# Kernel tuning notes

Hardware: AMD Instinct MI355X
Metric: run time of the kernel (lower is better)

## Reference

```python
import jax, jax.numpy as jnp
import numpy as np

N = 131072       # nodes
E = 2097152      # edges
B = 4096         # target user/item pairs (= batched subgraphs)
F_IN = 32        # dataset.num_features
H = 32           # latent dim per conv layer
L = 4            # num conv layers
R = 5            # num relations
NB = 4           # num bases
D = 256          # 2*sum(latent_dim), LSTM input/hidden size


def setup_inputs() -> dict:
    key = jax.random.key(0)
    ks = jax.random.split(key, 16)
    x = jax.random.normal(ks[0], (N, F_IN), dtype=jnp.float32)
    edge_index = jax.random.randint(ks[1], (2, E), 0, N, dtype=jnp.int32)
    edge_type = jax.random.randint(ks[2], (E,), 0, R, dtype=jnp.int32)
    user_idx = jnp.arange(B, dtype=jnp.int32)
    item_idx = jnp.arange(B, dtype=jnp.int32) + B
    s = 0.1
    basis = jax.random.normal(ks[3], (L, NB, H, H), dtype=jnp.float32) * s
    comp = jax.random.normal(ks[4], (L, R, NB), dtype=jnp.float32) * s
    root = jax.random.normal(ks[5], (L, H, H), dtype=jnp.float32) * s
    conv_bias = jnp.zeros((L, H), dtype=jnp.float32)
    w_ih = jax.random.normal(ks[6], (2, 4 * D, D), dtype=jnp.float32) * (1.0 / np.sqrt(D))
    w_hh = jax.random.normal(ks[7], (2, 4 * D, D), dtype=jnp.float32) * (1.0 / np.sqrt(D))
    b_ih = jnp.zeros((2, 4 * D), dtype=jnp.float32)
    b_hh = jnp.zeros((2, 4 * D), dtype=jnp.float32)
    lin1_w = jax.random.normal(ks[8], (128, D), dtype=jnp.float32) * (1.0 / np.sqrt(D))
    lin1_b = jnp.zeros((128,), dtype=jnp.float32)
    lin2_w = jax.random.normal(ks[9], (1, 128), dtype=jnp.float32) * (1.0 / np.sqrt(128))
    lin2_b = jnp.zeros((1,), dtype=jnp.float32)
    return dict(x=x, edge_index=edge_index, edge_type=edge_type,
                user_idx=user_idx, item_idx=item_idx,
                basis=basis, comp=comp, root=root, conv_bias=conv_bias,
                w_ih=w_ih, w_hh=w_hh, b_ih=b_ih, b_hh=b_hh,
                lin1_w=lin1_w, lin1_b=lin1_b, lin2_w=lin2_w, lin2_b=lin2_b)


def _lstm_layer(inp, w_ih_l, w_hh_l, b_ih_l, b_hh_l):
    # inp: [T, D] unbatched sequence (torch LSTM with 2D input)
    T = inp.shape[0]
    # precompute input contribution for all timesteps: [T, 4D]
    x_gates = inp @ w_ih_l.T + b_ih_l + b_hh_l

    def step(carry, xg):
        h, c = carry
        gates = xg + h @ w_hh_l.T            # [4D]
        i, f, g, o = jnp.split(gates, 4)
        i = jax.nn.sigmoid(i)
        f = jax.nn.sigmoid(f)
        g = jnp.tanh(g)
        o = jax.nn.sigmoid(o)
        c = f * c + i * g
        h = o * jnp.tanh(c)
        return (h, c), h

    h0 = jnp.zeros((D,), dtype=inp.dtype)
    (_, _), out = jax.lax.scan(step, (h0, h0), x_gates)
    return out  # [T, D]


def _forward(x, edge_index, edge_type, user_idx, item_idx,
             basis, comp, root, conv_bias,
             w_ih, w_hh, b_ih, b_hh, lin1_w, lin1_b, lin2_w, lin2_b):
    src, dst = edge_index[0], edge_index[1]
    # per-(dst, relation) mean normalization (RGCNConv aggr='mean'); same every layer
    seg = dst.astype(jnp.int32) * R + edge_type.astype(jnp.int32)  # [E]
    counts = jax.ops.segment_sum(jnp.ones((E,), jnp.float32), seg, num_segments=N * R)
    edge_norm = (1.0 / jnp.maximum(counts, 1.0))[seg]              # [E]

    h = x
    concat_states = []
    for l in range(L):
        # basis-decomposed relation weights: W_r = sum_b comp[r,b] * basis[b]
        basis_out = jnp.einsum('nd,bde->nbe', h, basis[l])         # [N, NB, H]
        comp_e = comp[l][edge_type]                                 # [E, NB]
        msg = jnp.einsum('eb,ebo->eo', comp_e, basis_out[src])      # [E, H]
        msg = msg * edge_norm[:, None]
        agg = jax.ops.segment_sum(msg, dst, num_segments=N)         # [N, H]
        h = jnp.tanh(agg + h @ root[l] + conv_bias[l])
        concat_states.append(h)
    states = jnp.concatenate(concat_states, axis=1)                 # [N, 4H] = [N,128]

    u = states[user_idx]                                            # [B, 128]
    v = states[item_idx]                                            # [B, 128]
    z = jnp.concatenate([u, v], axis=1)                             # [B, 256]

    # 2-layer LSTM over the B dimension (torch treats [B,256] as seq_len=B, unbatched)
    z = _lstm_layer(z, w_ih[0], w_hh[0], b_ih[0], b_hh[0])
    z = _lstm_layer(z, w_ih[1], w_hh[1], b_ih[1], b_hh[1])

    z = jax.nn.relu(z @ lin1_w.T + lin1_b)                          # [B, 128]
    z = z @ lin2_w.T + lin2_b                                       # [B, 1]
    return z[:, 0]


def reference(x, edge_index, edge_type, user_idx, item_idx,
              basis, comp, root, conv_bias,
              w_ih, w_hh, b_ih, b_hh, lin1_w, lin1_b, lin2_w, lin2_b):
    return _forward(x, edge_index, edge_type, user_idx, item_idx,
                    basis, comp, root, conv_bias,
                    w_ih, w_hh, b_ih, b_hh, lin1_w, lin1_b, lin2_w, lin2_b)
```

## Files before the change

kernel.cpp:

```cpp
#include <hip/hip_runtime.h>
#include <hip/hip_bf16.h>
#include <hip/hip_fp16.h>

#define N_NODES 131072
#define N_EDGES 2097152
#define BSZ     4096
#define NREL    5
#define NBASIS  4

typedef unsigned int uint;
typedef unsigned short ushort;
typedef _Float16 v2h __attribute__((ext_vector_type(2)));
typedef __attribute__((ext_vector_type(8))) short bf16x8;
typedef __attribute__((ext_vector_type(4))) float f32x4;
typedef uint u32x4v __attribute__((ext_vector_type(4)));

__device__ __forceinline__ float bflo(uint u){ union{uint i;float f;}x; x.i = u<<16; return x.f; }
__device__ __forceinline__ float bf2f(ushort u){ return bflo((uint)u); }
__device__ __forceinline__ ushort f2bf(float f){
  union{float f;uint i;}x; x.f=f;
  uint r = (x.i + 0x7fffu + ((x.i>>16)&1u)) >> 16;
  return (ushort)r;
}
__device__ __forceinline__ float sigm(float x){ return 1.0f/(1.0f+__expf(-x)); }
__device__ __forceinline__ float tanh_fast(float x){
  x = fminf(fmaxf(x,-15.f),15.f);
  float e = __expf(2.0f*x);
  return (e-1.0f)/(e+1.0f);
}
__device__ __forceinline__ float dot2h(uint a, uint b, float c){
#if __has_builtin(__builtin_amdgcn_fdot2)
  return __builtin_amdgcn_fdot2(__builtin_bit_cast(v2h,a), __builtin_bit_cast(v2h,b), c, false);
#else
  v2h ah = __builtin_bit_cast(v2h,a), bh = __builtin_bit_cast(v2h,b);
  return c + (float)ah.x*(float)bh.x + (float)ah.y*(float)bh.y;
#endif
}

__device__ __forceinline__ void store16(uint* p, u32x4v v){
  asm volatile("global_store_dwordx4 %0, %1, off sc0 sc1" :: "v"(p), "v"(v) : "memory");
}
__device__ __forceinline__ u32x4v poll16(const uint* p, uint want){
  u32x4v v;
  do {
    asm volatile("global_load_dwordx4 %0, %1, off sc0 sc1\n\ts_waitcnt vmcnt(0)"
      : "=v"(v) : "v"(p) : "memory");
  } while (v.x != want);
  return v;
}

__global__ void k_cvt_half(const float* __restrict__ in, __half* __restrict__ out, int n){
  int i = blockIdx.x*256 + threadIdx.x;
  if (i < n) out[i] = __float2half(in[i]);
}
__global__ void k_cvt_bf(const float* __restrict__ in, ushort* __restrict__ out, int n){
  int i = blockIdx.x*256 + threadIdx.x;
  if (i < n) out[i] = f2bf(in[i]);
}

__global__ void k_count(const int* __restrict__ ei, const int* __restrict__ et, int* __restrict__ cnt){
  int e = blockIdx.x*256 + threadIdx.x;
  if (e < N_EDGES){
    int d = ei[N_EDGES + e];
    int r = et[e];
    atomicAdd(&cnt[d*NREL + r], 1);
  }
}
__global__ void k_inv(float* __restrict__ buf){
  int i = blockIdx.x*256 + threadIdx.x;
  if (i < N_NODES*NREL){
    int c = ((int*)buf)[i];
    buf[i] = (c > 0) ? (1.0f/(float)c) : 1.0f;
  }
}

__global__ void k_hb(const float* __restrict__ x, const ushort* __restrict__ states, int l,
                     const float* __restrict__ basis_l, uint2* __restrict__ hb){
  __shared__ float bs[NBASIS*32*32];
  __shared__ float hs[256];
  int tid = threadIdx.x;
  #pragma unroll
  for (int r = 0; r < 16; r++){ int idx = r*256 + tid; bs[idx] = basis_l[idx]; }
  int nbase = blockIdx.x*8;
  if (l == 0){
    hs[tid] = x[nbase*32 + tid];
  } else {
    int n = nbase + (tid >> 5), i = tid & 31;
    hs[tid] = bf2f(states[n*128 + (l-1)*32 + i]);
  }
  __syncthreads();
  int nl = tid >> 5, j = tid & 31;
  float a0=0.f,a1=0.f,a2=0.f,a3=0.f;
  #pragma unroll
  for (int i = 0; i < 32; i++){
    float hv = hs[nl*32 + i];
    a0 += hv*bs[0*1024 + i*32 + j];
    a1 += hv*bs[1*1024 + i*32 + j];
    a2 += hv*bs[2*1024 + i*32 + j];
    a3 += hv*bs[3*1024 + i*32 + j];
  }
  uint2 o;
  o.x = (uint)f2bf(a0) | ((uint)f2bf(a1) << 16);
  o.y = (uint)f2bf(a2) | ((uint)f2bf(a3) << 16);
  hb[(nbase + nl)*32 + j] = o;
}

__global__ void k_edge(const int* __restrict__ ei, const int* __restrict__ et,
                       const float* __restrict__ comp_l, const float* __restrict__ inv,
                       const uint2* __restrict__ hb, float* __restrict__ agg){
  __shared__ float cl[NREL*NBASIS];
  int tid = threadIdx.x;
  if (tid < NREL*NBASIS) cl[tid] = comp_l[tid];
  __syncthreads();
  int e = blockIdx.x*8 + (tid >> 5);
  int j = tid & 31;
  int src = ei[e];
  int dst = ei[N_EDGES + e];
  int r = et[e];
  float nrm = inv[dst*NREL + r];
  uint2 v = hb[src*32 + j];
  float m = nrm*(cl[r*4+0]*bflo(v.x)       + cl[r*4+1]*bflo(v.x >> 16)
               + cl[r*4+2]*bflo(v.y)       + cl[r*4+3]*bflo(v.y >> 16));
  atomicAdd(&agg[dst*32 + j], m);
}

__global__ void k_combine(const float* __restrict__ agg, const float* __restrict__ x,
                          ushort* __restrict__ states, int l,
                          const float* __restrict__ root_l, const float* __restrict__ bias_l){
  __shared__ float rt[1024];
  __shared__ float hs[256];
  int tid = threadIdx.x;
  #pragma unroll
  for (int r = 0; r < 4; r++) rt[r*256 + tid] = root_l[r*256 + tid];
  int nbase = blockIdx.x*8;
  if (l == 0){
    hs[tid] = x[nbase*32 + tid];
  } else {
    int n = nbase + (tid >> 5), i = tid & 31;
    hs[tid] = bf2f(states[n*128 + (l-1)*32 + i]);
  }
  __syncthreads();
  int nl = tid >> 5, j = tid & 31;
  int n = nbase + nl;
  float acc = agg[n*32 + j] + bias_l[j];
  #pragma unroll
  for (int i = 0; i < 32; i++) acc += hs[nl*32 + i] * rt[i*32 + j];
  states[n*128 + l*32 + j] = f2bf(tanh_fast(acc));
}

__global__ void k_gather(const ushort* __restrict__ states, const int* __restrict__ uidx,
                         const int* __restrict__ vidx, ushort* __restrict__ z){
  int b = blockIdx.x;
  int k = threadIdx.x;
  int node = (k < 128) ? uidx[b] : vidx[b];
  z[b*256 + k] = states[node*128 + (k & 127)];
}

__global__ void k_xgemm(const ushort* __restrict__ A, const ushort* __restrict__ W,
                        const float* __restrict__ bih, const float* __restrict__ bhh,
                        float* __restrict__ xg){
  int gw = blockIdx.x*4 + (threadIdx.x >> 6);
  int lane = threadIdx.x & 63;
  int t0 = (gw >> 6)*16;
  int j0 = (gw & 63)*16;
  int m = lane & 15, q = lane >> 4;
  const ushort* ap = A + (t0 + m)*256 + q*8;
  const ushort* bp = W + (j0 + m)*256 + q*8;
  f32x4 acc = {0.f,0.f,0.f,0.f};
  #pragma unroll
  for (int kk = 0; kk < 8; kk++){
    bf16x8 a = *(const bf16x8*)(ap + kk*32);
    bf16x8 b = *(const bf16x8*)(bp + kk*32);
    acc = __builtin_amdgcn_mfma_f32_16x16x32_bf16(a, b, acc, 0, 0, 0);
  }
  int j = j0 + m;
  float bias = bih[j] + bhh[j];
  #pragma unroll
  for (int r = 0; r < 4; r++){
    int t = t0 + q*4 + r;
    xg[t*1024 + j] = acc[r] + bias;
  }
}

#define REP8J(M,q) M(q,0) M(q,1) M(q,2) M(q,3) M(q,4) M(q,5) M(q,6) M(q,7)
#define REPQ(M) REP8J(M,0) REP8J(M,1) REP8J(M,2) REP8J(M,3)
#define WDECL(q,j) uint4 W##q##_##j = wp##q[j];
#define WPIN(q,j)  asm volatile("" : "+v"(W##q##_##j.x), "+v"(W##q##_##j.y), \
                                     "+v"(W##q##_##j.z), "+v"(W##q##_##j.w));
#define DOTJ(j) { uint4 H = hp[j]; \
  a0 = dot2h(W0_##j.x, H.x, a0); b0 = dot2h(W0_##j.y, H.y, b0); \
  a0 = dot2h(W0_##j.z, H.z, a0); b0 = dot2h(W0_##j.w, H.w, b0); \
  a1 = dot2h(W1_##j.x, H.x, a1); b1 = dot2h(W1_##j.y, H.y, b1); \
  a1 = dot2h(W1_##j.z, H.z, a1); b1 = dot2h(W1_##j.w, H.w, b1); \
  a2 = dot2h(W2_##j.x, H.x, a2); b2 = dot2h(W2_##j.y, H.y, b2); \
  a2 = dot2h(W2_##j.z, H.z, a2); b2 = dot2h(W2_##j.w, H.w, b2); \
  a3 = dot2h(W3_##j.x, H.x, a3); b3 = dot2h(W3_##j.y, H.y, b3); \
  a3 = dot2h(W3_##j.z, H.z, a3); b3 = dot2h(W3_##j.w, H.w, b3); }
#define BFLY(r) { \
  float _t = __int_as_float(__builtin_amdgcn_update_dpp(0, __float_as_int(r), 0xB1, 0xF, 0xF, true)); \
  r += _t; \
  _t = __int_as_float(__builtin_amdgcn_update_dpp(0, __float_as_int(r), 0x4E, 0xF, 0xF, true)); \
  r += _t; }

__launch_bounds__(256, 1)
__global__ void k_scan4(const float* __restrict__ xg, const __half* __restrict__ whh,
                        ushort* __restrict__ outh, uint* hx){
  int b = blockIdx.x;
  if (b & 7) return;
  int g = b >> 3;
  if (g >= 4) return;
  __shared__ uint hq[2][144];
  int t = threadIdx.x;
  int w = t >> 6, lane = t & 63, qd = lane >> 2, s = lane & 3;
  int u = g*64 + w*16 + qd;
  const uint4* wp0 = (const uint4*)(whh + ((size_t)(u      ))*256 + s*64);
  const uint4* wp1 = (const uint4*)(whh + ((size_t)(u + 256))*256 + s*64);
  const uint4* wp2 = (const uint4*)(whh + ((size_t)(u + 512))*256 + s*64);
  const uint4* wp3 = (const uint4*)(whh + ((size_t)(u + 768))*256 + s*64);
  REPQ(WDECL)
  REPQ(WPIN)
  if (t < 144) hq[0][t] = 0u;
  float c = 0.f;
  float px = xg[s*256 + u];
  int pollidx = t - 64;
  int bb = (lane & 48) * 4;
  __syncthreads();
  for (int step = 0; step < 4096; step++){
    int rb = step & 1, wb = rb ^ 1;
    const uint4* hp = (const uint4*)&hq[rb][s*36];
    float a0=0.f,a1=0.f,a2=0.f,a3=0.f,b0=0.f,b1=0.f,b2=0.f,b3=0.f;
    int nstep = (step < 4095) ? step + 1 : step;
    float npx = xg[(size_t)nstep*1024 + s*256 + u];
    DOTJ(0) DOTJ(1) DOTJ(2) DOTJ(3) DOTJ(4) DOTJ(5) DOTJ(6) DOTJ(7)
    float r0 = a0 + b0, r1 = a1 + b1, r2 = a2 + b2, r3 = a3 + b3;
    r0 += (s == 0) ? px : 0.f;
    r1 += (s == 1) ? px : 0.f;
    r2 += (s == 2) ? px : 0.f;
    r3 += (s == 3) ? px : 0.f;
    BFLY(r0) BFLY(r1) BFLY(r2) BFLY(r3)
    float iv = sigm(r0), fv = sigm(r1), gv = tanh_fast(r2), ov = sigm(r3);
    c = fv*c + iv*gv;
    float hv = ov*tanh_fast(c);
    px = npx;
    uint hvh = (uint)__half_as_ushort(__float2half(hv));
    uint g0 = (uint)__builtin_amdgcn_ds_bpermute(bb +  0, (int)hvh);
    uint g1 = (uint)__builtin_amdgcn_ds_bpermute(bb + 16, (int)hvh);
    uint g2 = (uint)__builtin_amdgcn_ds_bpermute(bb + 32, (int)hvh);
    uint g3 = (uint)__builtin_amdgcn_ds_bpermute(bb + 48, (int)hvh);
    if ((lane & 15) == 0){
      int cc = w*4 + (lane >> 4);
      u32x4v ch;
      ch.x = (uint)(step + 1);
      ch.y = (g0 & 0xffffu) | (g1 << 16);
      ch.z = (g2 & 0xffffu) | (g3 << 16);
      ch.w = 0u;
      store16(hx + (((size_t)rb*4 + g)*16 + cc)*4, ch);
    }
    if (s == 0){
      ((__half*)&hq[wb][g*36])[w*16 + qd] = __ushort_as_half((ushort)hvh);
      outh[(size_t)step*256 + u] = f2bf(hv);
    }
    if ((uint)pollidx < 48u){
      int o = pollidx >> 4, cc = pollidx & 15;
      int gg = o + (o >= g);
      u32x4v v = poll16(hx + (((size_t)rb*4 + gg)*16 + cc)*4, (uint)(step + 1));
      hq[wb][gg*36 + 2*cc]     = v.y;
      hq[wb][gg*36 + 2*cc + 1] = v.z;
    }
    __syncthreads();
  }
}

__global__ void k_head1(const ushort* __restrict__ h, const float* __restrict__ w,
                        const float* __restrict__ b, float* __restrict__ out){
  __shared__ float s[256];
  int t = blockIdx.x, j = threadIdx.x;
  s[j]       = bf2f(h[t*256 + j]);
  s[j + 128] = bf2f(h[t*256 + 128 + j]);
  __syncthreads();
  float acc = b[j];
  const float4* wr4 = (const float4*)(w + j*256);
  #pragma unroll
  for (int k4 = 0; k4 < 64; k4++){
    float4 v = wr4[k4];
    int k = k4*4;
    acc += s[k+0]*v.x + s[k+1]*v.y + s[k+2]*v.z + s[k+3]*v.w;
  }
  out[t*128 + j] = fmaxf(acc, 0.f);
}
__global__ void k_head2(const float* __restrict__ hm, const float* __restrict__ w,
                        const float* __restrict__ b, float* __restrict__ out){
  int t = blockIdx.x*256 + threadIdx.x;
  if (t < BSZ){
    float acc = b[0];
    #pragma unroll
    for (int k = 0; k < 128; k++) acc += hm[t*128 + k]*w[k];
    out[t] = acc;
  }
}

extern "C" void kernel_launch(void* const* d_in, const int* in_sizes, int n_in,
                              void* d_out, int out_size, void* d_ws, size_t ws_size,
                              hipStream_t stream){
  const float* x     = (const float*)d_in[0];
  const int*   ei    = (const int*)d_in[1];
  const int*   et    = (const int*)d_in[2];
  const int*   uidx  = (const int*)d_in[3];
  const int*   vidx  = (const int*)d_in[4];
  const float* basis = (const float*)d_in[5];
  const float* comp  = (const float*)d_in[6];
  const float* root  = (const float*)d_in[7];
  const float* cbias = (const float*)d_in[8];
  const float* w_ih  = (const float*)d_in[9];
  const float* w_hh  = (const float*)d_in[10];
  const float* b_ih  = (const float*)d_in[11];
  const float* b_hh  = (const float*)d_in[12];
  const float* lin1w = (const float*)d_in[13];
  const float* lin1b = (const float*)d_in[14];
  const float* lin2w = (const float*)d_in[15];
  const float* lin2b = (const float*)d_in[16];

  char* ws = (char*)d_ws;
  __half* whh16  = (__half*)(ws + 0);
  ushort* wihbf  = (ushort*)(ws + 1048576);
  float*  inv    = (float*) (ws + 2097152);
  ushort* states = (ushort*)(ws + 4718592);
  char*   scr    = ws + 38273024;
  uint2*  hb     = (uint2*)(scr);
  float*  agg    = (float*)(scr + 33554432);
  ushort* z      = (ushort*)(scr + 0);
  ushort* out1   = (ushort*)(scr + 2097152);
  ushort* out2   = (ushort*)(scr + 4194304);
  float*  hmid   = (float*) (scr + 6291456);
  float*  xg     = (float*) (scr + 8388608);
  uint*   hx1    = (uint*)  (scr + 25165824);
  uint*   hx2    = (uint*)  (scr + 25167872);

  k_cvt_half<<<2048, 256, 0, stream>>>(w_hh, whh16, 2*1024*256);
  k_cvt_bf  <<<2048, 256, 0, stream>>>(w_ih, wihbf, 2*1024*256);
  hipMemsetAsync(inv, 0, (size_t)N_NODES*NREL*4, stream);
  k_count<<<N_EDGES/256, 256, 0, stream>>>(ei, et, (int*)inv);
  k_inv<<<(N_NODES*NREL)/256, 256, 0, stream>>>(inv);

  for (int l = 0; l < 4; l++){
    k_hb<<<N_NODES/8, 256, 0, stream>>>(x, states, l, basis + l*NBASIS*1024, hb);
    hipMemsetAsync(agg, 0, (size_t)N_NODES*32*4, stream);
    k_edge<<<N_EDGES/8, 256, 0, stream>>>(ei, et, comp + l*NREL*NBASIS, inv, hb, agg);
    k_combine<<<N_NODES/8, 256, 0, stream>>>(agg, x, states, l, root + l*1024, cbias + l*32);
  }

  k_gather<<<BSZ, 256, 0, stream>>>(states, uidx, vidx, z);
  k_xgemm<<<4096, 256, 0, stream>>>(z,    wihbf,          b_ih,        b_hh,        xg);
  k_scan4<<<25, 256, 0, stream>>>(xg, whh16,          out1, hx1);
  k_xgemm<<<4096, 256, 0, stream>>>(out1, wihbf + 262144, b_ih + 1024, b_hh + 1024, xg);
  k_scan4<<<25, 256, 0, stream>>>(xg, whh16 + 262144, out2, hx2);
  k_head1<<<BSZ, 128, 0, stream>>>(out2, lin1w, lin1b, hmid);
  k_head2<<<BSZ/256, 256, 0, stream>>>(hmid, lin2w, lin2b, (float*)d_out);
}
```

Baseline: 11.07 ms.

## Co-locate LSTM scan blocks on one XCC and sync through L2

The recurrent scan kernel now launches 64 blocks. Each block reads its XCC id and claims a rank through an atomic counter, so that four blocks sharing one XCC form the cooperating group. A handshake checks whether L2-scoped (sc0) stores are visible between those blocks; if they are, the per-step hidden-state exchange polls L2 instead of the system-coherent sc0|sc1 path. If the handshake fails or the spins run out, it falls back to the L3-coherent copy, and every store is written to both locations. This is meant to cut cross-die coherence latency on each of the 4096 serial steps, at the cost of extra stores, a startup handshake, and reliance on XCC scheduling behaviour.

Result: slower. 14.41 ms (+30.1%).

```diff
diff --git a/kernel.cpp b/kernel.cpp
--- a/kernel.cpp
+++ b/kernel.cpp
@@ -37,15 +37,22 @@
 #endif
 }
 
-__device__ __forceinline__ void store16(uint* p, u32x4v v){
+__device__ __forceinline__ void store16_l2(uint* p, u32x4v v){
+  asm volatile("global_store_dwordx4 %0, %1, off sc0" :: "v"(p), "v"(v) : "memory");
+}
+__device__ __forceinline__ void store16_l3(uint* p, u32x4v v){
   asm volatile("global_store_dwordx4 %0, %1, off sc0 sc1" :: "v"(p), "v"(v) : "memory");
 }
-__device__ __forceinline__ u32x4v poll16(const uint* p, uint want){
+__device__ __forceinline__ u32x4v load16_l2(const uint* p){
   u32x4v v;
-  do {
-    asm volatile("global_load_dwordx4 %0, %1, off sc0 sc1\n\ts_waitcnt vmcnt(0)"
-      : "=v"(v) : "v"(p) : "memory");
-  } while (v.x != want);
+  asm volatile("global_load_dwordx4 %0, %1, off sc0\n\ts_waitcnt vmcnt(0)"
+    : "=v"(v) : "v"(p) : "memory");
+  return v;
+}
+__device__ __forceinline__ u32x4v load16_l3(const uint* p){
+  u32x4v v;
+  asm volatile("global_load_dwordx4 %0, %1, off sc0 sc1\n\ts_waitcnt vmcnt(0)"
+    : "=v"(v) : "v"(p) : "memory");
   return v;
 }
 
@@ -205,12 +212,23 @@
 __launch_bounds__(256, 1)
 __global__ void k_scan4(const float* __restrict__ xg, const __half* __restrict__ whh,
                         ushort* __restrict__ outh, uint* hx){
-  int b = blockIdx.x;
-  if (b & 7) return;
-  int g = b >> 3;
-  if (g >= 4) return;
   __shared__ uint hq[2][144];
+  __shared__ uint srank, srgn, sflag;
   int t = threadIdx.x;
+  uint xcc;
+  asm volatile("s_getreg_b32 %0, hwreg(HW_REG_XCC_ID)" : "=s"(xcc));
+  uint* claim = hx + 16384;
+  if (t == 0){
+    uint rg = xcc & 7u;
+    srgn = rg;
+    srank = __hip_atomic_fetch_add(&claim[rg], 1u, __ATOMIC_RELAXED, __HIP_MEMORY_SCOPE_AGENT);
+  }
+  __syncthreads();
+  uint rank = srank, rgn = srgn;
+  if (rank >= 4u) return;
+  int g = (int)rank;
+  uint* R = hx + (size_t)rgn*2048;
+
   int w = t >> 6, lane = t & 63, qd = lane >> 2, s = lane & 3;
   int u = g*64 + w*16 + qd;
   const uint4* wp0 = (const uint4*)(whh + ((size_t)(u      ))*256 + s*64);
@@ -220,11 +238,38 @@
   REPQ(WDECL)
   REPQ(WPIN)
   if (t < 144) hq[0][t] = 0u;
+
+  if (t == 0){
+    u32x4v wm; wm.x = 0xA11CEu; wm.y = 0u; wm.z = 0u; wm.w = 0u;
+    store16_l2(R + 1024 + g*4, wm);
+    asm volatile("s_waitcnt vmcnt(0)" ::: "memory");
+    store16_l3(R + 1040 + g*4, wm);
+    uint mode = 1u;
+    for (int o = 0; o < 4 && mode != 2u; o++){
+      if (o == g) continue;
+      int spins = 0; u32x4v v;
+      for (;;){
+        v = load16_l3(R + 1040 + o*4);
+        if (v.x == 0xA11CEu) break;
+        if (++spins > 5000){ mode = 2u; break; }
+      }
+      if (mode != 2u){
+        u32x4v w2 = load16_l2(R + 1024 + o*4);
+        if (w2.x != 0xA11CEu) mode = 0u;
+      }
+    }
+    sflag = mode;
+  }
+  __syncthreads();
+  uint mode = sflag;
+  if (mode == 2u) return;
+  bool fastc = (mode == 1u);
+
   float c = 0.f;
   float px = xg[s*256 + u];
   int pollidx = t - 64;
   int bb = (lane & 48) * 4;
-  __syncthreads();
+
   for (int step = 0; step < 4096; step++){
     int rb = step & 1, wb = rb ^ 1;
     const uint4* hp = (const uint4*)&hq[rb][s*36];
@@ -254,7 +299,9 @@
       ch.y = (g0 & 0xffffu) | (g1 << 16);
       ch.z = (g2 & 0xffffu) | (g3 << 16);
       ch.w = 0u;
-      store16(hx + (((size_t)rb*4 + g)*16 + cc)*4, ch);
+      uint off = (((uint)rb*4 + (uint)g)*16 + (uint)cc)*4;
+      store16_l2(R + off, ch);
+      store16_l3(R + 512 + off, ch);
     }
     if (s == 0){
       ((__half*)&hq[wb][g*36])[w*16 + qd] = __ushort_as_half((ushort)hvh);
@@ -263,7 +310,18 @@
     if ((uint)pollidx < 48u){
       int o = pollidx >> 4, cc = pollidx & 15;
       int gg = o + (o >= g);
-      u32x4v v = poll16(hx + (((size_t)rb*4 + gg)*16 + cc)*4, (uint)(step + 1));
+      uint off = (((uint)rb*4 + (uint)gg)*16 + (uint)cc)*4;
+      uint want = (uint)(step + 1);
+      u32x4v v; bool got = false;
+      if (fastc){
+        int spins = 0;
+        do { v = load16_l2(R + off); if (v.x == want){ got = true; break; } }
+        while (++spins < 4096);
+        if (!got) fastc = false;
+      }
+      if (!got){
+        do { v = load16_l3(R + 512 + off); } while (v.x != want);
+      }
       hq[wb][gg*36 + 2*cc]     = v.y;
       hq[wb][gg*36 + 2*cc + 1] = v.z;
     }
@@ -334,7 +392,7 @@
   float*  hmid   = (float*) (scr + 6291456);
   float*  xg     = (float*) (scr + 8388608);
   uint*   hx1    = (uint*)  (scr + 25165824);
-  uint*   hx2    = (uint*)  (scr + 25167872);
+  uint*   hx2    = (uint*)  (scr + 25231616);
 
   k_cvt_half<<<2048, 256, 0, stream>>>(w_hh, whh16, 2*1024*256);
   k_cvt_bf  <<<2048, 256, 0, stream>>>(w_ih, wihbf, 2*1024*256);
@@ -351,9 +409,11 @@
 
   k_gather<<<BSZ, 256, 0, stream>>>(states, uidx, vidx, z);
   k_xgemm<<<4096, 256, 0, stream>>>(z,    wihbf,          b_ih,        b_hh,        xg);
-  k_scan4<<<25, 256, 0, stream>>>(xg, whh16,          out1, hx1);
+  hipMemsetAsync(hx1, 0, 65792, stream);
+  k_scan4<<<64, 256, 0, stream>>>(xg, whh16,          out1, hx1);
   k_xgemm<<<4096, 256, 0, stream>>>(out1, wihbf + 262144, b_ih + 1024, b_hh + 1024, xg);
-  k_scan4<<<25, 256, 0, stream>>>(xg, whh16 + 262144, out2, hx2);
+  hipMemsetAsync(hx2, 0, 65792, stream);
+  k_scan4<<<64, 256, 0, stream>>>(xg, whh16 + 262144, out2, hx2);
   k_head1<<<BSZ, 128, 0, stream>>>(out2, lin1w, lin1b, hmid);
   k_head2<<<BSZ/256, 256, 0, stream>>>(hmid, lin2w, lin2b, (float*)d_out);
 }
```
